# Optimization experiments

Hardware: AMD Instinct MI355X
Metric: run time of the kernel (lower is better)

The kernel has to match this reference:

```python
import jax, jax.numpy as jnp
import numpy as np
import math

NUM_LEAD = 12
PATCHES = 100  # patch_num_v * patch_num_h = 5 * 20
HEADS = 12
HID = 768
DH = HID // HEADS  # 64
SEQ = NUM_LEAD * PATCHES + NUM_LEAD + 1  # 1213
INTER = 3072
BATCH = 8


def _layer_norm(x, g, b, eps=1e-12):
    u = x.mean(-1, keepdims=True)
    s = ((x - u) ** 2).mean(-1, keepdims=True)
    return g * (x - u) / jnp.sqrt(s + eps) + b


def _lead_mask():
    # make_mask with fusion == 0: additive bias applied to query rows [0, NUM_LEAD+1)
    cols = jnp.arange(SEQ)
    # CLS row: 1 at lead-token positions 1..NUM_LEAD
    cls_row = jnp.where((cols >= 1) & (cols < NUM_LEAD + 1), 1.0, 0.0)
    # Lead rows: 1 everywhere except own patch block
    i = jnp.arange(NUM_LEAD)[:, None]
    start = NUM_LEAD + 1 + PATCHES * i
    in_block = (cols[None, :] >= start) & (cols[None, :] < start + PATCHES)
    lead_rows = jnp.where(in_block, 0.0, 1.0)
    mask = jnp.concatenate([cls_row[None, :], lead_rows], axis=0)  # [NUM_LEAD+1, SEQ]
    return mask * (-99999.0)


def setup_inputs() -> dict:
    key = jax.random.key(0)
    ks = jax.random.split(key, 12)
    std = 0.02
    d = {
        "hidden_states": jax.random.normal(ks[0], (BATCH, SEQ, HID), jnp.float32),
        "attention_mask": jnp.zeros((BATCH, 1, 1, SEQ), jnp.float32),
        "Wq": jax.random.normal(ks[1], (HID, HID), jnp.float32) * std,
        "bq": jnp.zeros((HID,), jnp.float32),
        "Wk": jax.random.normal(ks[2], (HID, HID), jnp.float32) * std,
        "bk": jnp.zeros((HID,), jnp.float32),
        "Wv": jax.random.normal(ks[3], (HID, HID), jnp.float32) * std,
        "bv": jnp.zeros((HID,), jnp.float32),
        "Wo": jax.random.normal(ks[4], (HID, HID), jnp.float32) * std,
        "bo": jnp.zeros((HID,), jnp.float32),
        "gamma1": jnp.ones((HID,), jnp.float32),
        "beta1": jnp.zeros((HID,), jnp.float32),
        "Wi": jax.random.normal(ks[5], (HID, INTER), jnp.float32) * std,
        "bi": jnp.zeros((INTER,), jnp.float32),
        "Wd": jax.random.normal(ks[6], (INTER, HID), jnp.float32) * std,
        "bd": jnp.zeros((HID,), jnp.float32),
        "gamma2": jnp.ones((HID,), jnp.float32),
        "beta2": jnp.zeros((HID,), jnp.float32),
    }
    return d


def reference(hidden_states, attention_mask, Wq, bq, Wk, bk, Wv, bv, Wo, bo,
              gamma1, beta1, Wi, bi, Wd, bd, gamma2, beta2):
    B, S, _ = hidden_states.shape

    def heads(x):  # [B,S,HID] -> [B,H,S,DH]
        return x.reshape(B, S, HEADS, DH).transpose(0, 2, 1, 3)

    q = heads(hidden_states @ Wq + bq)
    k = heads(hidden_states @ Wk + bk)
    v = heads(hidden_states @ Wv + bv)

    scores = jnp.einsum("bhqd,bhkd->bhqk", q, k) / math.sqrt(DH)
    scores = scores + attention_mask  # broadcast [B,1,1,S]
    lead_mask = _lead_mask()  # [NUM_LEAD+1, SEQ]
    scores = scores.at[:, :, : NUM_LEAD + 1, :].add(lead_mask[None, None])

    probs = jax.nn.softmax(scores, axis=-1)  # dropout is identity in eval
    ctx = jnp.einsum("bhqk,bhkd->bhqd", probs, v)
    ctx = ctx.transpose(0, 2, 1, 3).reshape(B, S, HID)

    attn_out = _layer_norm(ctx @ Wo + bo + hidden_states, gamma1, beta1)
    inter = jax.nn.gelu(attn_out @ Wi + bi, approximate=False)  # exact erf gelu
    out = _layer_norm(inter @ Wd + bd + attn_out, gamma2, beta2)
    return out
```

## Files before the change

### kernel.cpp

```cpp
#include <hip/hip_runtime.h>
#include <hip/hip_bf16.h>
#include <stdint.h>

typedef unsigned short u16;
typedef unsigned int u32;
typedef __attribute__((ext_vector_type(8))) short frag8;
typedef __attribute__((ext_vector_type(4))) float f32x4;

#define SEQ 1213
#define SEQP 1216
#define BATCH 8
#define HEADS 12
#define DH 64
#define HID 768
#define INTER 3072
#define BS (BATCH*SEQ)
#define LOG2E 1.44269504088896f

#define MFMA(a,b,c) __builtin_amdgcn_mfma_f32_16x16x32_bf16(a,b,c,0,0,0)

__device__ __forceinline__ float b2f(u16 u){ u32 i=((u32)u)<<16; float f; __builtin_memcpy(&f,&i,4); return f; }
__device__ __forceinline__ u16 f2b(float f){ u32 i; __builtin_memcpy(&i,&f,4); i = i + 0x7fffu + ((i>>16)&1u); return (u16)(i>>16); }

__device__ __forceinline__ void async16(const u16* g, u16* l){
  __builtin_amdgcn_global_load_lds((const __attribute__((address_space(1))) u32*)(uintptr_t)g,
                                   (__attribute__((address_space(3))) u32*)(uintptr_t)l, 16, 0, 0);
}

__global__ __launch_bounds__(256) void convert_arr(const void* __restrict__ src,
  u16* __restrict__ dst, int n8, const u16* __restrict__ probe)
{
  const bool f32 = (probe[0] == 0);
  int i = blockIdx.x*256 + threadIdx.x;
  if (i >= n8) return;
  u16 tmp[8];
  if (f32){
    const float* s = (const float*)src + (size_t)i*8;
#pragma unroll
    for (int j=0;j<8;j++) tmp[j] = f2b(s[j]);
  } else {
    *(uint4*)tmp = *((const uint4*)src + i);
  }
  *((uint4*)dst + i) = *(const uint4*)tmp;
}

__global__ __launch_bounds__(256) void convert_small(
  const void* bq, const void* bk, const void* bv, const void* bo,
  const void* bi, const void* bd, const void* g1, const void* be1,
  const void* g2, const void* be2, const void* am,
  u16* __restrict__ dst, const u16* __restrict__ probe)
{
  const int starts[12] = {0,768,1536,2304,3072,6144,6912,7680,8448,9216,9984,19688};
  const void* srcs[11] = {bq,bk,bv,bo,bi,bd,g1,be1,g2,be2,am};
  const bool f32 = (probe[0] == 0);
  int e = (blockIdx.x*256 + threadIdx.x) * 8;
  if (e >= 19688) return;
  int seg = 0;
#pragma unroll
  for (int k=1;k<11;k++) if (starts[k] <= e) seg = k;
  int off = e - starts[seg];
  const void* s = srcs[seg];
  u16 tmp[8];
  if (f32){
    const float* sf = (const float*)s + off;
#pragma unroll
    for (int j=0;j<8;j++) tmp[j] = f2b(sf[j]);
  } else {
    const u16* sh = (const u16*)s + off;
#pragma unroll
    for (int j=0;j<8;j++) tmp[j] = sh[j];
  }
  *(uint4*)(dst + e) = *(const uint4*)tmp;
}

__global__ __launch_bounds__(256) void transpose2(const void* __restrict__ in,
  u16* __restrict__ out, int R, int C, const u16* __restrict__ probe)
{
  const bool f32 = (probe[0] == 0);
  __shared__ u16 tile[32][33];
  const int bx = blockIdx.x*32, by = blockIdx.y*32;
  const int tx = threadIdx.x & 31, ty = threadIdx.x >> 5;
  if (f32){
    const float* inf_ = (const float*)in;
#pragma unroll
    for (int i=ty;i<32;i+=8) tile[i][tx] = f2b(inf_[(size_t)(by+i)*C + bx+tx]);
  } else {
    const u16* inh = (const u16*)in;
#pragma unroll
    for (int i=ty;i<32;i+=8) tile[i][tx] = inh[(size_t)(by+i)*C + bx+tx];
  }
  __syncthreads();
#pragma unroll
  for (int i=ty;i<32;i+=8) out[(size_t)(bx+i)*R + by+tx] = tile[tx][i];
}

__global__ __launch_bounds__(256) void vtrans(const u16* __restrict__ V, u16* __restrict__ VT)
{
  __shared__ u16 tile[32][33];
  const int bh = blockIdx.z;
  const int s0 = blockIdx.x*32;
  const int d0 = blockIdx.y*32;
  const int tx = threadIdx.x & 31, ty = threadIdx.x >> 5;
  const u16* Vp = V + (size_t)bh*SEQ*64;
  u16* Tp = VT + (size_t)bh*64*SEQP;
#pragma unroll
  for (int i=ty;i<32;i+=8){
    int s = s0 + i;
    tile[i][tx] = (s < SEQ) ? Vp[(size_t)s*64 + d0 + tx] : (u16)0;
  }
  __syncthreads();
#pragma unroll
  for (int i=ty;i<32;i+=8)
    Tp[(size_t)(d0 + i)*SEQP + s0 + tx] = tile[tx][i];
}

__device__ __forceinline__ void gemm_tile(
    const u16* __restrict__ A, const u16* __restrict__ BT,
    int M, int K, int m0, int n0,
    u16* ldsA, u16* ldsB, f32x4 acc[4][4])
{
  const int t = threadIdx.x;
  const int w = t >> 6, l = t & 63;
  const int lw = l & 15, lh = l >> 4;
  const int rowo = (w >> 1) << 6;
  const int colo = (w & 1) << 6;
  const int srow = w*8 + (l>>3);
  const int scol = ((l&7) ^ ((l>>3)&7)) * 8;

  const u16* gpA[4]; const u16* gpB[4];
  u16* lpA[4]; u16* lpB[4];
#pragma unroll
  for (int p=0;p<4;p++){
    int ra = m0 + p*32 + srow; if (ra >= M) ra = M-1;
    gpA[p] = A  + (size_t)ra*K + scol;
    gpB[p] = BT + (size_t)(n0 + p*32 + srow)*K + scol;
    lpA[p] = ldsA + (p*32 + w*8)*64 + l*8;
    lpB[p] = ldsB + (p*32 + w*8)*64 + l*8;
  }

  const int slot0 = lw & 7;
  for (int k0 = 0; k0 < K; k0 += 64) {
    __syncthreads();
#pragma unroll
    for (int p=0;p<4;p++) async16(gpA[p] + k0, lpA[p]);
#pragma unroll
    for (int p=0;p<4;p++) async16(gpB[p] + k0, lpB[p]);
    __syncthreads();
#pragma unroll
    for (int kk=0;kk<2;kk++){
      const int slot = ((kk*4 + lh) ^ slot0) * 8;
      frag8 af[4], bf[4];
#pragma unroll
      for (int mi=0;mi<4;mi++) af[mi] = *(const frag8*)(ldsA + (rowo + mi*16 + lw)*64 + slot);
#pragma unroll
      for (int ni=0;ni<4;ni++) bf[ni] = *(const frag8*)(ldsB + (colo + ni*16 + lw)*64 + slot);
#pragma unroll
      for (int mi=0;mi<4;mi++)
#pragma unroll
        for (int ni=0;ni<4;ni++)
          acc[mi][ni] = MFMA(af[mi], bf[ni], acc[mi][ni]);
    }
  }
}

__global__ __launch_bounds__(256,2) void gemm_qkv(
  const u16* __restrict__ A, const u16* __restrict__ BT,
  const u16* __restrict__ bq, const u16* __restrict__ bk, const u16* __restrict__ bv,
  u16* __restrict__ Qo, u16* __restrict__ Ko, u16* __restrict__ Vo)
{
  __shared__ __align__(16) u16 ldsA[128*64];
  __shared__ __align__(16) u16 ldsB[128*64];
  f32x4 acc[4][4];
#pragma unroll
  for (int i=0;i<4;i++)
#pragma unroll
    for (int j=0;j<4;j++) acc[i][j] = 0.f;
  const int m0 = blockIdx.x*128, n0 = blockIdx.y*128;
  gemm_tile(A, BT, BS, HID, m0, n0, ldsA, ldsB, acc);
  const int t=threadIdx.x, w=t>>6, l=t&63, lw=l&15, lh=l>>4;
  const int rowb = m0 + ((w>>1)<<6), colb = n0 + ((w&1)<<6);
#pragma unroll
  for (int ni=0;ni<4;ni++){
    int cc = colb + ni*16 + lw;
    int which = cc / HID;
    int n2 = cc - which*HID;
    int h = n2 >> 6, d = n2 & 63;
    const u16* bp = which==0 ? bq : (which==1 ? bk : bv);
    u16* op = which==0 ? Qo : (which==1 ? Ko : Vo);
    float bias = b2f(bp[n2]);
    float scale = which==0 ? 0.125f : 1.0f;
#pragma unroll
    for (int mi=0;mi<4;mi++){
#pragma unroll
      for (int r=0;r<4;r++){
        int rr = rowb + mi*16 + lh*4 + r;
        if (rr < BS){
          int bi_ = rr / SEQ;
          int si  = rr - bi_*SEQ;
          float v = (acc[mi][ni][r] + bias) * scale;
          op[(((size_t)(bi_*HEADS + h))*SEQ + si)*64 + d] = f2b(v);
        }
      }
    }
  }
}

__global__ __launch_bounds__(256,2) void gemm_resid(
  const u16* __restrict__ A, const u16* __restrict__ BT,
  const u16* __restrict__ bias, const u16* __restrict__ resid,
  u16* __restrict__ out, int N, int K)
{
  __shared__ __align__(16) u16 ldsA[128*64];
  __shared__ __align__(16) u16 ldsB[128*64];
  f32x4 acc[4][4];
#pragma unroll
  for (int i=0;i<4;i++)
#pragma unroll
    for (int j=0;j<4;j++) acc[i][j] = 0.f;
  const int m0 = blockIdx.x*128, n0 = blockIdx.y*128;
  gemm_tile(A, BT, BS, K, m0, n0, ldsA, ldsB, acc);
  const int t=threadIdx.x, w=t>>6, l=t&63, lw=l&15, lh=l>>4;
  const int rowb = m0 + ((w>>1)<<6), colb = n0 + ((w&1)<<6);
#pragma unroll
  for (int ni=0;ni<4;ni++){
    int cc = colb + ni*16 + lw;
    float bv_ = b2f(bias[cc]);
#pragma unroll
    for (int mi=0;mi<4;mi++){
#pragma unroll
      for (int r=0;r<4;r++){
        int rr = rowb + mi*16 + lh*4 + r;
        if (rr < BS){
          float v = acc[mi][ni][r] + bv_ + b2f(resid[(size_t)rr*N + cc]);
          out[(size_t)rr*N + cc] = f2b(v);
        }
      }
    }
  }
}

__global__ __launch_bounds__(256,2) void gemm_gelu(
  const u16* __restrict__ A, const u16* __restrict__ BT,
  const u16* __restrict__ bias, u16* __restrict__ out, int N, int K)
{
  __shared__ __align__(16) u16 ldsA[128*64];
  __shared__ __align__(16) u16 ldsB[128*64];
  f32x4 acc[4][4];
#pragma unroll
  for (int i=0;i<4;i++)
#pragma unroll
    for (int j=0;j<4;j++) acc[i][j] = 0.f;
  const int m0 = blockIdx.x*128, n0 = blockIdx.y*128;
  gemm_tile(A, BT, BS, K, m0, n0, ldsA, ldsB, acc);
  const int t=threadIdx.x, w=t>>6, l=t&63, lw=l&15, lh=l>>4;
  const int rowb = m0 + ((w>>1)<<6), colb = n0 + ((w&1)<<6);
#pragma unroll
  for (int ni=0;ni<4;ni++){
    int cc = colb + ni*16 + lw;
    float bv_ = b2f(bias[cc]);
#pragma unroll
    for (int mi=0;mi<4;mi++){
#pragma unroll
      for (int r=0;r<4;r++){
        int rr = rowb + mi*16 + lh*4 + r;
        if (rr < BS){
          float v = acc[mi][ni][r] + bv_;
          v = 0.5f * v * (1.0f + erff(v * 0.70710678118654752f));
          out[(size_t)rr*N + cc] = f2b(v);
        }
      }
    }
  }
}

__global__ __launch_bounds__(512,1) void attn_kernel(
  const u16* __restrict__ Qb, const u16* __restrict__ Kb, const u16* __restrict__ Vt,
  const u16* __restrict__ amask, u16* __restrict__ ctx)
{
  __shared__ __align__(16) u16 sQP[128*72];
  __shared__ __align__(16) u16 sK[2][64*72];
  __shared__ __align__(16) u16 sV[2][64*64];
  __shared__ float sEm[2][64];
  const int t = threadIdx.x, w = t>>6, l = t&63, lw = l&15, lh = l>>4;
  const int bh = blockIdx.y, b = bh / HEADS;
  const int q0 = blockIdx.x * 128;
  const size_t hb = (size_t)bh * SEQ * 64;
  const u16* Qp = Qb + hb;
  const u16* Kp = Kb + hb;
  const u16* Vp = Vt + (size_t)bh * 64 * SEQP;

  const int rr = t >> 3, c = t & 7;
  const int wsw = ((c ^ (rr&7))<<3);
  const int cc0 = (lw&7) ^ lh;

  {
#pragma unroll
    for (int i=0;i<2;i++){
      int qr = i*64 + rr;
      int s = q0 + qr; if (s > SEQ-1) s = SEQ-1;
      *(uint4*)(sQP + qr*72 + c*8) = *(const uint4*)(Qp + (size_t)s*64 + c*8);
    }
  }

  uint4 kreg, vreg; float emreg = 0.f;
  {
    kreg = *(const uint4*)(Kp + (size_t)rr*64 + c*8);
    vreg = *(const uint4*)(Vp + (size_t)rr*SEQP + c*8);
    if (t < 64) emreg = b2f(amask[b*SEQ + t]) * LOG2E;
  }
  __syncthreads();

  frag8 qa[2];
#pragma unroll
  for (int kk=0;kk<2;kk++) qa[kk] = *(const frag8*)(sQP + (w*16 + lw)*72 + kk*32 + lh*8);

  *(uint4*)(&sK[0][rr*72 + c*8]) = kreg;
  *(uint4*)(&sV[0][rr*64 + wsw]) = vreg;
  if (t < 64) sEm[0][t] = emreg;
  __syncthreads();

  float l_p = 0.f;
  f32x4 o[4];
#pragma unroll
  for (int i=0;i<4;i++) o[i] = 0.f;
  const bool leadwave = (q0 == 0) && (w == 0);

  const int nkt = (SEQ + 63) / 64;
  for (int kt = 0; kt < nkt; kt++) {
    const int p = kt & 1;
    const u16* sKp = sK[p];
    const u16* sVp = sV[p];
    const float* sEp = sEm[p];
    const bool pf_next = (kt+1 < nkt);
    if (pf_next){
      int s = (kt+1)*64 + rr; if (s > SEQ-1) s = SEQ-1;
      kreg = *(const uint4*)(Kp + (size_t)s*64 + c*8);
      vreg = *(const uint4*)(Vp + (size_t)rr*SEQP + (kt+1)*64 + c*8);
      if (t < 64){
        int sg = (kt+1)*64 + t;
        emreg = (sg < SEQ) ? b2f(amask[b*SEQ + sg]) * LOG2E : -1e30f;
      }
    }

    f32x4 st[4];
#pragma unroll
    for (int si=0;si<4;si++){
      f32x4 a0 = 0.f;
#pragma unroll
      for (int kk=0;kk<2;kk++){
        frag8 kf = *(const frag8*)(sKp + (si*16 + lw)*72 + kk*32 + lh*8);
        a0 = MFMA(kf, qa[kk], a0);
      }
      st[si] = a0;
    }

#pragma unroll
    for (int si=0;si<4;si++){
      f32x4 emv = *(const f32x4*)(sEp + si*16 + lh*4);
#pragma unroll
      for (int r=0;r<4;r++)
        st[si][r] = exp2f(fmaf(st[si][r], LOG2E, emv[r]));
    }
    if (leadwave){
#pragma unroll
      for (int si=0;si<4;si++){
#pragma unroll
        for (int r=0;r<4;r++){
          int sg = kt*64 + si*16 + lh*4 + r;
          int q = lw;
          float pv = st[si][r];
          if (q == 0){
            if (sg >= 1 && sg < 13) pv = 0.f;
          } else if (q < 13){
            int stt = 13 + 100*(q-1);
            if (!(sg >= stt && sg < stt+100)) pv = 0.f;
          }
          st[si][r] = pv;
        }
      }
    }
#pragma unroll
    for (int si=0;si<4;si++)
#pragma unroll
      for (int r=0;r<4;r++) l_p += st[si][r];

    u32 pa[4], pb[4];
#pragma unroll
    for (int si=0;si<4;si++){
      asm("v_cvt_pk_bf16_f32 %0, %1, %2" : "=v"(pa[si]) : "v"(st[si][0]), "v"(st[si][1]));
      asm("v_cvt_pk_bf16_f32 %0, %1, %2" : "=v"(pb[si]) : "v"(st[si][2]), "v"(st[si][3]));
    }
    asm("v_permlane32_swap_b32 %0, %1" : "+v"(pa[0]), "+v"(pa[1]));
    asm("v_permlane32_swap_b32 %0, %1" : "+v"(pa[2]), "+v"(pa[3]));
    asm("v_permlane32_swap_b32 %0, %1" : "+v"(pb[0]), "+v"(pb[1]));
    asm("v_permlane32_swap_b32 %0, %1" : "+v"(pb[2]), "+v"(pb[3]));
    asm("v_permlane16_swap_b32 %0, %1" : "+v"(pa[0]), "+v"(pa[1]));
    asm("v_permlane16_swap_b32 %0, %1" : "+v"(pa[2]), "+v"(pa[3]));
    asm("v_permlane16_swap_b32 %0, %1" : "+v"(pb[0]), "+v"(pb[1]));
    asm("v_permlane16_swap_b32 %0, %1" : "+v"(pb[2]), "+v"(pb[3]));

#pragma unroll
    for (int kk=0;kk<2;kk++){
      union { u32 u[4]; frag8 f; } pfu;
      pfu.u[0] = pa[kk*2+0]; pfu.u[1] = pb[kk*2+0];
      pfu.u[2] = pa[kk*2+1]; pfu.u[3] = pb[kk*2+1];
      frag8 pf = pfu.f;
#pragma unroll
      for (int ni=0;ni<4;ni++){
        frag8 vf = *(const frag8*)(sVp + (ni*16+lw)*64 + ((cc0 ^ (kk<<2))<<3));
        o[ni] = MFMA(pf, vf, o[ni]);
      }
    }

    if (pf_next){
      const int pn = p ^ 1;
      *(uint4*)(&sK[pn][rr*72 + c*8]) = kreg;
      *(uint4*)(&sV[pn][rr*64 + wsw]) = vreg;
      if (t < 64) sEm[pn][t] = emreg;
      __syncthreads();
    }
  }

  l_p += __shfl_xor(l_p, 16);
  l_p += __shfl_xor(l_p, 32);

  const int h = bh % HEADS;
#pragma unroll
  for (int r=0;r<4;r++){
    float lf = __shfl(l_p, (l & 48) + ((l >> 4) << 2) + r);
    int qg = q0 + w*16 + lh*4 + r;
    if (qg < SEQ){
      float inv = 1.0f / lf;
#pragma unroll
      for (int ni=0;ni<4;ni++){
        ctx[((size_t)(b*SEQ) + qg)*HID + h*64 + ni*16 + lw] = f2b(o[ni][r] * inv);
      }
    }
  }
}

__global__ __launch_bounds__(256) void ln_kernel(const u16* __restrict__ y,
  const u16* __restrict__ g, const u16* __restrict__ be,
  u16* __restrict__ outb, float* __restrict__ outf)
{
  const int row = blockIdx.x, t = threadIdx.x;
  const u16* yp = y + (size_t)row*HID;
  float x0 = b2f(yp[t]), x1 = b2f(yp[t+256]), x2 = b2f(yp[t+512]);
  float s = x0 + x1 + x2;
  __shared__ float red[4];
#pragma unroll
  for (int off=1; off<64; off<<=1) s += __shfl_xor(s, off);
  if ((t & 63) == 0) red[t>>6] = s;
  __syncthreads();
  float u = (red[0]+red[1]+red[2]+red[3]) * (1.0f/768.0f);
  float d0=x0-u, d1=x1-u, d2=x2-u;
  float s2 = d0*d0 + d1*d1 + d2*d2;
  __syncthreads();
#pragma unroll
  for (int off=1; off<64; off<<=1) s2 += __shfl_xor(s2, off);
  if ((t & 63) == 0) red[t>>6] = s2;
  __syncthreads();
  float var = (red[0]+red[1]+red[2]+red[3]) * (1.0f/768.0f);
  float rstd = rsqrtf(var + 1e-12f);
  float v0 = b2f(g[t])    *(d0*rstd) + b2f(be[t]);
  float v1 = b2f(g[t+256])*(d1*rstd) + b2f(be[t+256]);
  float v2 = b2f(g[t+512])*(d2*rstd) + b2f(be[t+512]);
  if (outf){
    float* op = outf + (size_t)row*HID;
    op[t] = v0; op[t+256] = v1; op[t+512] = v2;
  } else {
    u16* op = outb + (size_t)row*HID;
    op[t] = f2b(v0); op[t+256] = f2b(v1); op[t+512] = f2b(v2);
  }
}

extern "C" void kernel_launch(void* const* d_in, const int* in_sizes, int n_in,
                              void* d_out, int out_size, void* d_ws, size_t ws_size,
                              hipStream_t stream)
{
  const void* hidden = d_in[0];
  const void* amask  = d_in[1];
  const void* Wq = d_in[2];  const void* bq = d_in[3];
  const void* Wk = d_in[4];  const void* bk = d_in[5];
  const void* Wv = d_in[6];  const void* bv = d_in[7];
  const void* Wo = d_in[8];  const void* bo = d_in[9];
  const void* g1 = d_in[10]; const void* be1= d_in[11];
  const void* Wi = d_in[12]; const void* bi = d_in[13];
  const void* Wd = d_in[14]; const void* bd = d_in[15];
  const void* g2 = d_in[16]; const void* be2= d_in[17];
  const u16* probe = (const u16*)g1;

  char* ws = (char*)d_ws;
  size_t off = 0;
  auto alloc = [&](size_t elems)->u16* {
    u16* p = (u16*)(ws + off);
    off += ((elems*2 + 255) & ~(size_t)255);
    return p;
  };
  u16* hiddenC = alloc((size_t)BS*HID);
  u16* smallC  = alloc((size_t)19688);
  u16* WqkvT = alloc((size_t)2304*768);
  u16* WoT   = alloc((size_t)768*768);
  u16* WiT   = alloc((size_t)3072*768);
  u16* WdT   = alloc((size_t)768*3072);
  u16* Qb    = alloc((size_t)BS*HID);
  u16* Kb    = alloc((size_t)BS*HID);
  u16* VTb   = alloc((size_t)BS*HID);
  u16* y1    = alloc((size_t)BS*HID);
  u16* interb = Qb;
  u16* ctxb  = alloc((size_t)BS*HID);
  u16* attn_out = alloc((size_t)BS*HID);
  u16* y2 = ctxb;
  u16* Vb = ctxb;

  const u16* c_bq = smallC;        const u16* c_bk = smallC+768;
  const u16* c_bv = smallC+1536;   const u16* c_bo = smallC+2304;
  const u16* c_bi = smallC+3072;   const u16* c_bd = smallC+6144;
  const u16* c_g1 = smallC+6912;   const u16* c_be1= smallC+7680;
  const u16* c_g2 = smallC+8448;   const u16* c_be2= smallC+9216;
  const u16* c_am = smallC+9984;

  dim3 blk(256);
  convert_arr<<<dim3((BS*HID/8 + 255)/256), blk, 0, stream>>>(hidden, hiddenC, BS*HID/8, probe);
  convert_small<<<dim3(10), blk, 0, stream>>>(bq,bk,bv,bo,bi,bd,g1,be1,g2,be2,amask, smallC, probe);
  transpose2<<<dim3(24,24),blk,0,stream>>>(Wq, WqkvT,              768, 768, probe);
  transpose2<<<dim3(24,24),blk,0,stream>>>(Wk, WqkvT + 768*768,    768, 768, probe);
  transpose2<<<dim3(24,24),blk,0,stream>>>(Wv, WqkvT + 2*768*768,  768, 768, probe);
  transpose2<<<dim3(24,24),blk,0,stream>>>(Wo, WoT, 768, 768, probe);
  transpose2<<<dim3(96,24),blk,0,stream>>>(Wi, WiT, 768, 3072, probe);
  transpose2<<<dim3(24,96),blk,0,stream>>>(Wd, WdT, 3072, 768, probe);

  gemm_qkv<<<dim3(76,18),blk,0,stream>>>(hiddenC, WqkvT, c_bq,c_bk,c_bv, Qb,Kb,Vb);
  vtrans<<<dim3(38,2,96),blk,0,stream>>>(Vb, VTb);
  attn_kernel<<<dim3(10,96),dim3(512),0,stream>>>(Qb,Kb,VTb, c_am, ctxb);
  gemm_resid<<<dim3(76,6),blk,0,stream>>>(ctxb, WoT, c_bo, hiddenC, y1, 768, 768);
  ln_kernel<<<dim3(BS),blk,0,stream>>>(y1, c_g1, c_be1, attn_out, nullptr);
  gemm_gelu<<<dim3(76,24),blk,0,stream>>>(attn_out, WiT, c_bi, interb, 3072, 768);
  gemm_resid<<<dim3(76,6),blk,0,stream>>>(interb, WdT, c_bd, attn_out, y2, 768, 3072);
  ln_kernel<<<dim3(BS),blk,0,stream>>>(y2, c_g2, c_be2, nullptr, (float*)d_out);
}
```

Before: 509.9 us.

## Use 256x256 double-buffered pipelined GEMM for QKV and GELU projections

Replaces the 128x128 single-buffered GEMM for the QKV and intermediate (GELU) projections with a 256x256-tile, 512-thread kernel. It double-buffers A/B tiles in LDS and interleaves async global-to-LDS loads with MFMA phases, using explicit vmcnt waits, raw barriers and s_setprio. This aims to raise operand reuse and hide load latency behind compute. In exchange it uses 128KB of LDS per block and far fewer blocks (342 and 456), which risks low occupancy and wave quantization on the 256-CU device.

After: 541.6 us. 6.2% more time.

```diff
diff --git a/kernel.cpp b/kernel.cpp
--- a/kernel.cpp
+++ b/kernel.cpp
@@ -27,6 +27,10 @@
                                    (__attribute__((address_space(3))) u32*)(uintptr_t)l, 16, 0, 0);
 }
 
+#define VMCNT6 asm volatile("s_waitcnt vmcnt(6)" ::: "memory")
+#define VMCNT0 asm volatile("s_waitcnt vmcnt(0)" ::: "memory")
+#define GBAR do{ asm volatile("" ::: "memory"); __builtin_amdgcn_s_barrier(); asm volatile("" ::: "memory"); }while(0)
+
 __global__ __launch_bounds__(256) void convert_arr(const void* __restrict__ src,
   u16* __restrict__ dst, int n8, const u16* __restrict__ probe)
 {
@@ -114,71 +118,118 @@
     Tp[(size_t)(d0 + i)*SEQP + s0 + tx] = tile[tx][i];
 }
 
-__device__ __forceinline__ void gemm_tile(
-    const u16* __restrict__ A, const u16* __restrict__ BT,
-    int M, int K, int m0, int n0,
-    u16* ldsA, u16* ldsB, f32x4 acc[4][4])
-{
-  const int t = threadIdx.x;
-  const int w = t >> 6, l = t & 63;
-  const int lw = l & 15, lh = l >> 4;
-  const int rowo = (w >> 1) << 6;
-  const int colo = (w & 1) << 6;
-  const int srow = w*8 + (l>>3);
-  const int scol = ((l&7) ^ ((l>>3)&7)) * 8;
-
-  const u16* gpA[4]; const u16* gpB[4];
-  u16* lpA[4]; u16* lpB[4];
-#pragma unroll
-  for (int p=0;p<4;p++){
-    int ra = m0 + p*32 + srow; if (ra >= M) ra = M-1;
-    gpA[p] = A  + (size_t)ra*K + scol;
-    gpB[p] = BT + (size_t)(n0 + p*32 + srow)*K + scol;
-    lpA[p] = ldsA + (p*32 + w*8)*64 + l*8;
-    lpB[p] = ldsB + (p*32 + w*8)*64 + l*8;
-  }
-
-  const int slot0 = lw & 7;
-  for (int k0 = 0; k0 < K; k0 += 64) {
-    __syncthreads();
-#pragma unroll
-    for (int p=0;p<4;p++) async16(gpA[p] + k0, lpA[p]);
-#pragma unroll
-    for (int p=0;p<4;p++) async16(gpB[p] + k0, lpB[p]);
-    __syncthreads();
-#pragma unroll
-    for (int kk=0;kk<2;kk++){
-      const int slot = ((kk*4 + lh) ^ slot0) * 8;
-      frag8 af[4], bf[4];
-#pragma unroll
-      for (int mi=0;mi<4;mi++) af[mi] = *(const frag8*)(ldsA + (rowo + mi*16 + lw)*64 + slot);
-#pragma unroll
-      for (int ni=0;ni<4;ni++) bf[ni] = *(const frag8*)(ldsB + (colo + ni*16 + lw)*64 + slot);
-#pragma unroll
-      for (int mi=0;mi<4;mi++)
-#pragma unroll
-        for (int ni=0;ni<4;ni++)
-          acc[mi][ni] = MFMA(af[mi], bf[ni], acc[mi][ni]);
-    }
-  }
-}
-
-__global__ __launch_bounds__(256,2) void gemm_qkv(
+
+__device__ __forceinline__ void g256_phase(
+  int q, int wm, int wn, int lw, int lh, int sw,
+  const u16* lA, const u16* lB, frag8 bfr[2][4], f32x4 acc[8][4],
+  const u16* gs0, u16* ld0, const u16* gs1, u16* ld1)
+{
+  if (q == 0){
+#pragma unroll
+    for (int kk=0;kk<2;kk++)
+#pragma unroll
+      for (int ni=0;ni<4;ni++)
+        bfr[kk][ni] = *(const frag8*)(lB + (wn*64 + ni*16 + lw)*64 + (((kk*4+lh) ^ sw)<<3));
+  }
+  frag8 af[2][2];
+#pragma unroll
+  for (int mm=0;mm<2;mm++)
+#pragma unroll
+    for (int kk=0;kk<2;kk++)
+      af[mm][kk] = *(const frag8*)(lA + (wm*128 + (q*2+mm)*16 + lw)*64 + (((kk*4+lh) ^ sw)<<3));
+  if (gs0){ async16(gs0, ld0); async16(gs1, ld1); }
+  __builtin_amdgcn_s_setprio(1);
+#pragma unroll
+  for (int mm=0;mm<2;mm++)
+#pragma unroll
+    for (int ni=0;ni<4;ni++)
+#pragma unroll
+      for (int kk=0;kk<2;kk++)
+        acc[q*2+mm][ni] = MFMA(af[mm][kk], bfr[kk][ni], acc[q*2+mm][ni]);
+  __builtin_amdgcn_s_setprio(0);
+}
+
+__device__ __forceinline__ void g256_main(const u16* __restrict__ A, const u16* __restrict__ BT,
+  int M, int K, int m0, int n0, u16* ldsA0, u16* ldsA1, u16* ldsB0, u16* ldsB1,
+  f32x4 acc[8][4])
+{
+  const int t = threadIdx.x, w = t>>6, l = t&63, lw = l&15, lh = l>>4;
+  const int wm = w>>2, wn = w&3;
+  const int sw = lw & 7;
+  const int sr = t>>3;
+  const int c8 = ((t&7) ^ (sr&7))*8;
+  const u16* pA[4]; const u16* pB[4]; int dof[4];
+#pragma unroll
+  for (int h=0;h<2;h++)
+#pragma unroll
+    for (int hf=0;hf<2;hf++){
+      int r = h*64 + hf*128 + sr;
+      int ra = m0 + r; if (ra >= M) ra = M-1;
+      pA[h*2+hf] = A  + (size_t)ra*K + c8;
+      pB[h*2+hf] = BT + (size_t)(n0 + r)*K + c8;
+      dof[h*2+hf] = r*64 + (t&7)*8;
+    }
+  frag8 bfr[2][4];
+
+  async16(pA[0], ldsA0+dof[0]); async16(pA[1], ldsA0+dof[1]);
+  async16(pA[2], ldsA0+dof[2]); async16(pA[3], ldsA0+dof[3]);
+  async16(pB[0], ldsB0+dof[0]); async16(pB[1], ldsB0+dof[1]);
+  async16(pB[2], ldsB0+dof[2]); async16(pB[3], ldsB0+dof[3]);
+  async16(pB[0]+64, ldsB1+dof[0]); async16(pB[1]+64, ldsB1+dof[1]);
+  async16(pB[2]+64, ldsB1+dof[2]); async16(pB[3]+64, ldsB1+dof[3]);
+  async16(pA[0]+64, ldsA1+dof[0]); async16(pA[1]+64, ldsA1+dof[1]);
+
+  const int nit = K/128;
+#pragma unroll 1
+  for (int it = 0; it < nit; ++it){
+    const int k0 = it*128;
+    const bool has2 = (k0 + 128 < K);
+    const bool has3 = (k0 + 192 < K);
+    const int kn = k0 + 128, kn3 = k0 + 192;
+    VMCNT6; GBAR;
+    g256_phase(0, wm, wn, lw, lh, sw, ldsA0, ldsB0, bfr, acc,
+               pA[2]+k0+64, ldsA1+dof[2], pA[3]+k0+64, ldsA1+dof[3]);
+    GBAR;
+    g256_phase(1, wm, wn, lw, lh, sw, ldsA0, ldsB0, bfr, acc,
+               has2? pB[0]+kn : (const u16*)0, ldsB0+dof[0], pB[1]+kn, ldsB0+dof[1]);
+    GBAR;
+    g256_phase(2, wm, wn, lw, lh, sw, ldsA0, ldsB0, bfr, acc,
+               has2? pB[2]+kn : (const u16*)0, ldsB0+dof[2], pB[3]+kn, ldsB0+dof[3]);
+    GBAR;
+    g256_phase(3, wm, wn, lw, lh, sw, ldsA0, ldsB0, bfr, acc,
+               has2? pA[0]+kn : (const u16*)0, ldsA0+dof[0], pA[1]+kn, ldsA0+dof[1]);
+    if (it == nit-1) { VMCNT0; } else { VMCNT6; }
+    GBAR;
+    g256_phase(0, wm, wn, lw, lh, sw, ldsA1, ldsB1, bfr, acc,
+               has2? pA[2]+kn : (const u16*)0, ldsA0+dof[2], pA[3]+kn, ldsA0+dof[3]);
+    GBAR;
+    g256_phase(1, wm, wn, lw, lh, sw, ldsA1, ldsB1, bfr, acc,
+               has3? pB[0]+kn3 : (const u16*)0, ldsB1+dof[0], pB[1]+kn3, ldsB1+dof[1]);
+    GBAR;
+    g256_phase(2, wm, wn, lw, lh, sw, ldsA1, ldsB1, bfr, acc,
+               has3? pB[2]+kn3 : (const u16*)0, ldsB1+dof[2], pB[3]+kn3, ldsB1+dof[3]);
+    GBAR;
+    g256_phase(3, wm, wn, lw, lh, sw, ldsA1, ldsB1, bfr, acc,
+               has3? pA[0]+kn3 : (const u16*)0, ldsA1+dof[0], pA[1]+kn3, ldsA1+dof[1]);
+  }
+}
+
+__global__ __launch_bounds__(512,2) void gemm256_qkv(
   const u16* __restrict__ A, const u16* __restrict__ BT,
   const u16* __restrict__ bq, const u16* __restrict__ bk, const u16* __restrict__ bv,
   u16* __restrict__ Qo, u16* __restrict__ Ko, u16* __restrict__ Vo)
 {
-  __shared__ __align__(16) u16 ldsA[128*64];
-  __shared__ __align__(16) u16 ldsB[128*64];
-  f32x4 acc[4][4];
-#pragma unroll
-  for (int i=0;i<4;i++)
+  __shared__ __align__(16) u16 ldsA[2][256*64];
+  __shared__ __align__(16) u16 ldsB[2][256*64];
+  f32x4 acc[8][4];
+#pragma unroll
+  for (int i=0;i<8;i++)
 #pragma unroll
     for (int j=0;j<4;j++) acc[i][j] = 0.f;
-  const int m0 = blockIdx.x*128, n0 = blockIdx.y*128;
-  gemm_tile(A, BT, BS, HID, m0, n0, ldsA, ldsB, acc);
+  const int m0 = blockIdx.x*256, n0 = blockIdx.y*256;
+  g256_main(A, BT, BS, HID, m0, n0, ldsA[0], ldsA[1], ldsB[0], ldsB[1], acc);
   const int t=threadIdx.x, w=t>>6, l=t&63, lw=l&15, lh=l>>4;
-  const int rowb = m0 + ((w>>1)<<6), colb = n0 + ((w&1)<<6);
+  const int rowb = m0 + (w>>2)*128, colb = n0 + (w&3)*64;
 #pragma unroll
   for (int ni=0;ni<4;ni++){
     int cc = colb + ni*16 + lw;
@@ -190,7 +241,7 @@
     float bias = b2f(bp[n2]);
     float scale = which==0 ? 0.125f : 1.0f;
 #pragma unroll
-    for (int mi=0;mi<4;mi++){
+    for (int mi=0;mi<8;mi++){
 #pragma unroll
       for (int r=0;r<4;r++){
         int rr = rowb + mi*16 + lh*4 + r;
@@ -205,6 +256,89 @@
   }
 }
 
+__global__ __launch_bounds__(512,2) void gemm256_gelu(
+  const u16* __restrict__ A, const u16* __restrict__ BT,
+  const u16* __restrict__ bias, u16* __restrict__ out, int N, int K)
+{
+  __shared__ __align__(16) u16 ldsA[2][256*64];
+  __shared__ __align__(16) u16 ldsB[2][256*64];
+  f32x4 acc[8][4];
+#pragma unroll
+  for (int i=0;i<8;i++)
+#pragma unroll
+    for (int j=0;j<4;j++) acc[i][j] = 0.f;
+  const int m0 = blockIdx.x*256, n0 = blockIdx.y*256;
+  g256_main(A, BT, BS, K, m0, n0, ldsA[0], ldsA[1], ldsB[0], ldsB[1], acc);
+  const int t=threadIdx.x, w=t>>6, l=t&63, lw=l&15, lh=l>>4;
+  const int rowb = m0 + (w>>2)*128, colb = n0 + (w&3)*64;
+#pragma unroll
+  for (int ni=0;ni<4;ni++){
+    int cc = colb + ni*16 + lw;
+    float bv_ = b2f(bias[cc]);
+#pragma unroll
+    for (int mi=0;mi<8;mi++){
+#pragma unroll
+      for (int r=0;r<4;r++){
+        int rr = rowb + mi*16 + lh*4 + r;
+        if (rr < BS){
+          float v = acc[mi][ni][r] + bv_;
+          v = 0.5f * v * (1.0f + erff(v * 0.70710678118654752f));
+          out[(size_t)rr*N + cc] = f2b(v);
+        }
+      }
+    }
+  }
+}
+
+__device__ __forceinline__ void gemm_tile(
+    const u16* __restrict__ A, const u16* __restrict__ BT,
+    int M, int K, int m0, int n0,
+    u16* ldsA, u16* ldsB, f32x4 acc[4][4])
+{
+  const int t = threadIdx.x;
+  const int w = t >> 6, l = t & 63;
+  const int lw = l & 15, lh = l >> 4;
+  const int rowo = (w >> 1) << 6;
+  const int colo = (w & 1) << 6;
+  const int srow = w*8 + (l>>3);
+  const int scol = ((l&7) ^ ((l>>3)&7)) * 8;
+
+  const u16* gpA[4]; const u16* gpB[4];
+  u16* lpA[4]; u16* lpB[4];
+#pragma unroll
+  for (int p=0;p<4;p++){
+    int ra = m0 + p*32 + srow; if (ra >= M) ra = M-1;
+    gpA[p] = A  + (size_t)ra*K + scol;
+    gpB[p] = BT + (size_t)(n0 + p*32 + srow)*K + scol;
+    lpA[p] = ldsA + (p*32 + w*8)*64 + l*8;
+    lpB[p] = ldsB + (p*32 + w*8)*64 + l*8;
+  }
+
+  const int slot0 = lw & 7;
+  for (int k0 = 0; k0 < K; k0 += 64) {
+    __syncthreads();
+#pragma unroll
+    for (int p=0;p<4;p++) async16(gpA[p] + k0, lpA[p]);
+#pragma unroll
+    for (int p=0;p<4;p++) async16(gpB[p] + k0, lpB[p]);
+    __syncthreads();
+#pragma unroll
+    for (int kk=0;kk<2;kk++){
+      const int slot = ((kk*4 + lh) ^ slot0) * 8;
+      frag8 af[4], bf[4];
+#pragma unroll
+      for (int mi=0;mi<4;mi++) af[mi] = *(const frag8*)(ldsA + (rowo + mi*16 + lw)*64 + slot);
+#pragma unroll
+      for (int ni=0;ni<4;ni++) bf[ni] = *(const frag8*)(ldsB + (colo + ni*16 + lw)*64 + slot);
+#pragma unroll
+      for (int mi=0;mi<4;mi++)
+#pragma unroll
+        for (int ni=0;ni<4;ni++)
+          acc[mi][ni] = MFMA(af[mi], bf[ni], acc[mi][ni]);
+    }
+  }
+}
+
 __global__ __launch_bounds__(256,2) void gemm_resid(
   const u16* __restrict__ A, const u16* __restrict__ BT,
   const u16* __restrict__ bias, const u16* __restrict__ resid,
@@ -232,40 +366,6 @@
         int rr = rowb + mi*16 + lh*4 + r;
         if (rr < BS){
           float v = acc[mi][ni][r] + bv_ + b2f(resid[(size_t)rr*N + cc]);
-          out[(size_t)rr*N + cc] = f2b(v);
-        }
-      }
-    }
-  }
-}
-
-__global__ __launch_bounds__(256,2) void gemm_gelu(
-  const u16* __restrict__ A, const u16* __restrict__ BT,
-  const u16* __restrict__ bias, u16* __restrict__ out, int N, int K)
-{
-  __shared__ __align__(16) u16 ldsA[128*64];
-  __shared__ __align__(16) u16 ldsB[128*64];
-  f32x4 acc[4][4];
-#pragma unroll
-  for (int i=0;i<4;i++)
-#pragma unroll
-    for (int j=0;j<4;j++) acc[i][j] = 0.f;
-  const int m0 = blockIdx.x*128, n0 = blockIdx.y*128;
-  gemm_tile(A, BT, BS, K, m0, n0, ldsA, ldsB, acc);
-  const int t=threadIdx.x, w=t>>6, l=t&63, lw=l&15, lh=l>>4;
-  const int rowb = m0 + ((w>>1)<<6), colb = n0 + ((w&1)<<6);
-#pragma unroll
-  for (int ni=0;ni<4;ni++){
-    int cc = colb + ni*16 + lw;
-    float bv_ = b2f(bias[cc]);
-#pragma unroll
-    for (int mi=0;mi<4;mi++){
-#pragma unroll
-      for (int r=0;r<4;r++){
-        int rr = rowb + mi*16 + lh*4 + r;
-        if (rr < BS){
-          float v = acc[mi][ni][r] + bv_;
-          v = 0.5f * v * (1.0f + erff(v * 0.70710678118654752f));
           out[(size_t)rr*N + cc] = f2b(v);
         }
       }
@@ -530,12 +630,12 @@
   transpose2<<<dim3(96,24),blk,0,stream>>>(Wi, WiT, 768, 3072, probe);
   transpose2<<<dim3(24,96),blk,0,stream>>>(Wd, WdT, 3072, 768, probe);
 
-  gemm_qkv<<<dim3(76,18),blk,0,stream>>>(hiddenC, WqkvT, c_bq,c_bk,c_bv, Qb,Kb,Vb);
+  gemm256_qkv<<<dim3(38,9),dim3(512),0,stream>>>(hiddenC, WqkvT, c_bq,c_bk,c_bv, Qb,Kb,Vb);
   vtrans<<<dim3(38,2,96),blk,0,stream>>>(Vb, VTb);
   attn_kernel<<<dim3(10,96),dim3(512),0,stream>>>(Qb,Kb,VTb, c_am, ctxb);
   gemm_resid<<<dim3(76,6),blk,0,stream>>>(ctxb, WoT, c_bo, hiddenC, y1, 768, 768);
   ln_kernel<<<dim3(BS),blk,0,stream>>>(y1, c_g1, c_be1, attn_out, nullptr);
-  gemm_gelu<<<dim3(76,24),blk,0,stream>>>(attn_out, WiT, c_bi, interb, 3072, 768);
+  gemm256_gelu<<<dim3(38,12),dim3(512),0,stream>>>(attn_out, WiT, c_bi, interb, 3072, 768);
   gemm_resid<<<dim3(76,6),blk,0,stream>>>(interb, WdT, c_bd, attn_out, y2, 768, 3072);
   ln_kernel<<<dim3(BS),blk,0,stream>>>(y2, c_g2, c_be2, nullptr, (float*)d_out);
 }
```
